# Kernel optimization log

Hardware: AMD Instinct MI355X
Metric: run time of the kernel (lower is better)

Reference implementation:

```python
import jax, jax.numpy as jnp
import numpy as np

N_TAYLOR = 4

def taylor_exp_poly(x, n_terms):
    # sum_{p=0}^{n_terms-1} x^p / p!  via Horner: 1 + x*(1 + x/2*(1 + x/3*(...)))
    acc = jnp.ones_like(x)
    for p in range(n_terms - 1, 0, -1):
        acc = 1.0 + (x / p) * acc
    return acc

def setup_inputs() -> dict:
    key = jax.random.key(0)
    kq, kk, kv = jax.random.split(key, 3)
    B, H, T, d_key, d_val = 4, 8, 2048, 32, 64
    Q = jax.random.normal(kq, (B, H, T, d_key), dtype=jnp.float32)
    K = jax.random.normal(kk, (B, H, T, d_key), dtype=jnp.float32)
    V = jax.random.normal(kv, (B, H, T, d_val), dtype=jnp.float32)
    return {"Q": Q, "K": K, "V": V}

def reference(Q, K, V):
    # Symmetry-aware Taylor-approximated attention (Heinsen & Kozachkov).
    # The tightly-packed degree-p feature maps phi_p satisfy
    #   phi_p(q) . phi_p(k) == (q.k / sqrt(d_key))^p / p!
    # so summing S/Z over all n_taylor terms equals attention with kernel
    #   w(q,k) = sum_{p<n_taylor} (q.k/sqrt(d_key))^p / p!   (truncated exp),
    # causally masked and normalized by the row-sum Z.
    d_key = Q.shape[-1]
    scale = 1.0 / jnp.sqrt(jnp.asarray(d_key, dtype=Q.dtype))
    scores = jnp.einsum('bhqd,bhkd->bhqk', Q, K) * scale  # [B,H,T,T]
    A = taylor_exp_poly(scores, N_TAYLOR)
    T = Q.shape[-2]
    causal = jnp.tril(jnp.ones((T, T), dtype=bool))  # [T,T]
    A = jnp.where(causal, A, jnp.zeros((), dtype=A.dtype))
    Z = jnp.sum(A, axis=-1, keepdims=True)           # [B,H,T,1]
    S = jnp.einsum('bhqk,bhkd->bhqd', A, V)          # [B,H,T,d_val]
    return S / Z
```

## Files before the change

### kernel.cpp

```cpp
#include <hip/hip_runtime.h>
#include <hip/hip_bf16.h>


typedef __attribute__((ext_vector_type(8))) short bf16x8;
typedef __attribute__((ext_vector_type(8))) _Float16 f16x8;
typedef __attribute__((ext_vector_type(2))) _Float16 h2;
typedef __attribute__((ext_vector_type(2))) __fp16 fp16x2b;
typedef __attribute__((ext_vector_type(4))) float f32x4;
typedef __attribute__((ext_vector_type(16))) float f32x16;
typedef unsigned int u32;
typedef unsigned short u16;

namespace {

constexpr int T_SEQ = 2048;
constexpr int DK    = 32;
constexpr int DV    = 64;
constexpr int NBH   = 32;

constexpr float C1 = 0.17677669529663687f;
constexpr float C2 = 0.015625f;
constexpr float C3 = 9.2071195e-4f;

constexpr size_t KHF_OFF  = 0;
constexpr size_t VTHF_OFF = (size_t)NBH * T_SEQ * DK * 2;
constexpr size_t WS_NEED  = VTHF_OFF + (size_t)NBH * DV * T_SEQ * 2;

__device__ __forceinline__ u32 pack_hi2(float f0, float f1) {
  return (__float_as_uint(f0) >> 16) | (__float_as_uint(f1) & 0xffff0000u);
}
__device__ __forceinline__ float trunc_bf(float f) {
  return __uint_as_float(__float_as_uint(f) & 0xffff0000u);
}
__device__ __forceinline__ u16 f2h(float f) {
  union { _Float16 h; u16 u; } c;
  c.h = (_Float16)f;
  return c.u;
}
__device__ __forceinline__ void permswap(u32& a, u32& b) {
  asm volatile("v_permlane32_swap_b32 %0, %1" : "+v"(a), "+v"(b));
}


__global__ void pack_kv(const float* __restrict__ Kg, const float* __restrict__ Vg,
                        u16* __restrict__ Khf, u16* __restrict__ Vthf) {
  __shared__ float tile[DV][33];
  const int bid = blockIdx.x;
  const int t   = threadIdx.x;
  if (bid < 2048) {
    size_t i = ((size_t)bid * 256 + t) * 4;
    float4 f = *(const float4*)(Kg + i);
    ushort4 h;
    h.x = f2h(f.x); h.y = f2h(f.y); h.z = f2h(f.z); h.w = f2h(f.w);
    *(ushort4*)(Khf + i) = h;
  } else {
    const int vb = bid - 2048;
    const int bh = vb >> 6;
    const int k0 = (vb & 63) * 32;
    {
      const int kl = t >> 3, c0 = (t & 7) * 8;
      const float* src = Vg + ((size_t)bh * T_SEQ + k0 + kl) * DV + c0;
      float4 a = *(const float4*)src;
      float4 b = *(const float4*)(src + 4);
      tile[c0 + 0][kl] = a.x; tile[c0 + 1][kl] = a.y;
      tile[c0 + 2][kl] = a.z; tile[c0 + 3][kl] = a.w;
      tile[c0 + 4][kl] = b.x; tile[c0 + 5][kl] = b.y;
      tile[c0 + 6][kl] = b.z; tile[c0 + 7][kl] = b.w;
    }
    __syncthreads();
    {
      const int cl = t >> 2, k8 = (t & 3) * 8;
      ushort4 h0, h1;
      h0.x = f2h(tile[cl][k8 + 0]); h0.y = f2h(tile[cl][k8 + 1]);
      h0.z = f2h(tile[cl][k8 + 2]); h0.w = f2h(tile[cl][k8 + 3]);
      h1.x = f2h(tile[cl][k8 + 4]); h1.y = f2h(tile[cl][k8 + 5]);
      h1.z = f2h(tile[cl][k8 + 6]); h1.w = f2h(tile[cl][k8 + 7]);
      size_t off = ((size_t)(bh * DV + cl)) * T_SEQ + k0 + k8;
      *(ushort4*)(Vthf + off)     = h0;
      *(ushort4*)(Vthf + off + 4) = h1;
    }
  }
}


__global__ __launch_bounds__(256, 4)
void taylor_attn_v10(const float* __restrict__ Qg, const u16* __restrict__ Khf,
                     const u16* __restrict__ Vthf, float* __restrict__ Outg) {
  __shared__ __align__(16) float Sp[4 * 2048];
  __shared__ float Zp[4 * 32];

  const int tid = threadIdx.x;
  const int l   = tid & 63;
  const int w   = tid >> 6;
  const int cq  = l & 31;
  const int hi  = l >> 5;

  const int bid = blockIdx.x;
  const int xcd = bid & 7;
  const int r_  = bid >> 3;
  const int bh  = xcd * 4 + (r_ & 3);
  const int p   = r_ >> 2;

  const u16* kq = Khf + (size_t)bh * T_SEQ * DK + (size_t)cq * DK + hi * 8;
  const u16* vq = Vthf + (size_t)bh * DV * T_SEQ + (size_t)cq * T_SEQ + hi * 8;
  const float* qb = Qg + (size_t)bh * T_SEQ * DK;

  const h2 C3h = {(_Float16)C3, (_Float16)C3};
  const h2 C2h = {(_Float16)C2, (_Float16)C2};
  const h2 C1h = {(_Float16)C1, (_Float16)C1};
  const h2 ONEh = {(_Float16)1.0f, (_Float16)1.0f};

  f32x16 ZERO;
#pragma unroll
  for (int r = 0; r < 16; ++r) ZERO[r] = 0.f;

#pragma unroll 1
  for (int ph = 0; ph < 2; ++ph) {
    const int s  = ph ? (63 - p) : p;
    const int q0 = s * 32;

    if (ph) __syncthreads();

    f16x8 qf[2];
#pragma unroll
    for (int t = 0; t < 2; ++t) {
      const float* qp = qb + (size_t)(q0 + cq) * DK + t * 16 + hi * 8;
      float4 a = *(const float4*)qp;
      float4 b = *(const float4*)(qp + 4);
      f16x8 v;
      v[0] = (_Float16)a.x; v[1] = (_Float16)a.y;
      v[2] = (_Float16)a.z; v[3] = (_Float16)a.w;
      v[4] = (_Float16)b.x; v[5] = (_Float16)b.y;
      v[6] = (_Float16)b.z; v[7] = (_Float16)b.w;
      qf[t] = v;
    }

    f32x16 acc0 = ZERO, acc1 = ZERO;
    float zacc = 0.f;

    auto LOADK = [&](f16x8* kf, int kt) {
      const u16* kp = kq + (size_t)kt * 1024;
      kf[0] = *(const f16x8*)kp;
      kf[1] = *(const f16x8*)(kp + 16);
    };
    auto LOADV = [&](f16x8* vf, int kt) {
#pragma unroll
      for (int ct = 0; ct < 2; ++ct)
#pragma unroll
        for (int t = 0; t < 2; ++t)
          vf[ct * 2 + t] = *(const f16x8*)(
              vq + (size_t)ct * 32 * T_SEQ + kt * 32 + t * 16);
    };
    auto STEP = [&](const f16x8* kf, const f16x8* vf, bool diag) {
      f32x16 d = __builtin_amdgcn_mfma_f32_32x32x16_f16(kf[0], qf[0], ZERO, 0, 0, 0);
      d = __builtin_amdgcn_mfma_f32_32x32x16_f16(kf[1], qf[1], d, 0, 0, 0);

      union cvu { fp16x2b p; h2 h; u32 u; };
      cvu wv[8];
#pragma unroll
      for (int j = 0; j < 8; ++j) {
        cvu c;
        c.p = __builtin_amdgcn_cvt_pkrtz(d[2 * j], d[2 * j + 1]);
        h2 sc = c.h;
        h2 t_ = sc * C3h + C2h;
        t_    = sc * t_ + C1h;
        wv[j].h = sc * t_ + ONEh;
      }
      if (diag) {
#pragma unroll
        for (int j = 0; j < 8; ++j) {
          const int r0   = 2 * j;
          const int kre  = (r0 & 3) + 8 * (r0 >> 2) + 4 * hi;
          u32 msk = ((kre <= cq) ? 0xffffu : 0u) |
                    ((kre + 1 <= cq) ? 0xffff0000u : 0u);
          wv[j].u &= msk;
        }
      }
      {
        h2 zs = ((wv[0].h + wv[1].h) + (wv[2].h + wv[3].h)) +
                ((wv[4].h + wv[5].h) + (wv[6].h + wv[7].h));
        zacc += (float)zs[0] + (float)zs[1];
      }
      union { f16x8 v; u32 u[4]; } WH[2];
#pragma unroll
      for (int t = 0; t < 2; ++t) {
        u32 p0 = wv[4 * t + 0].u, p1 = wv[4 * t + 1].u;
        u32 p2 = wv[4 * t + 2].u, p3 = wv[4 * t + 3].u;
        permswap(p0, p2); permswap(p1, p3);
        WH[t].u[0] = p0; WH[t].u[1] = p1; WH[t].u[2] = p2; WH[t].u[3] = p3;
      }
      acc0 = __builtin_amdgcn_mfma_f32_32x32x16_f16(WH[0].v, vf[0], acc0, 0, 0, 0);
      acc0 = __builtin_amdgcn_mfma_f32_32x32x16_f16(WH[1].v, vf[1], acc0, 0, 0, 0);
      acc1 = __builtin_amdgcn_mfma_f32_32x32x16_f16(WH[0].v, vf[2], acc1, 0, 0, 0);
      acc1 = __builtin_amdgcn_mfma_f32_32x32x16_f16(WH[1].v, vf[3], acc1, 0, 0, 0);
    };

    {
      int kt = w;
      if (kt < s) {
        f16x8 kA[2], kB[2];
        LOADK(kA, kt);
        while (true) {
          int kn = kt + 4;
          if (kn < s) {
            LOADK(kB, kn);
            f16x8 vf[4]; LOADV(vf, kt);
            STEP(kA, vf, false);
            kt = kn;
          } else {
            f16x8 vf[4]; LOADV(vf, kt);
            STEP(kA, vf, false);
            break;
          }
          kn = kt + 4;
          if (kn < s) {
            LOADK(kA, kn);
            f16x8 vf[4]; LOADV(vf, kt);
            STEP(kB, vf, false);
            kt = kn;
          } else {
            f16x8 vf[4]; LOADV(vf, kt);
            STEP(kB, vf, false);
            break;
          }
        }
      }
    }
    if ((s & 3) == w) {
      f16x8 kD[2]; LOADK(kD, s);
      f16x8 vD[4]; LOADV(vD, s);
      STEP(kD, vD, true);
    }

    {
      float zt = zacc + __shfl_xor(zacc, 32);
      if (hi == 0) Zp[w * 32 + cq] = zt;
    }
#pragma unroll
    for (int r = 0; r < 16; ++r) {
      const int qr = (r & 3) + 8 * (r >> 2) + 4 * hi;
      Sp[w * 2048 + qr * 64 + cq]      = acc0[r];
      Sp[w * 2048 + qr * 64 + 32 + cq] = acc1[r];
    }
    __syncthreads();

    const f32x4* S4 = (const f32x4*)Sp;
#pragma unroll
    for (int i = 0; i < 2; ++i) {
      const int e4  = tid + i * 256;
      const int row = e4 >> 4;
      f32x4 ssum = S4[e4] + S4[512 + e4] + S4[1024 + e4] + S4[1536 + e4];
      float z = Zp[row] + Zp[32 + row] + Zp[64 + row] + Zp[96 + row];
      float inv = 1.0f / z;
      float4 o;
      o.x = ssum[0] * inv; o.y = ssum[1] * inv;
      o.z = ssum[2] * inv; o.w = ssum[3] * inv;
      *(float4*)(Outg + ((size_t)bh * T_SEQ + q0 + row) * DV + (e4 & 15) * 4) = o;
    }
  }
}


constexpr int QT_FB = 64;
constexpr int KT_FB = 32;
constexpr int LDSW  = 40;
constexpr float SCALE = 0.17677669529663687f;

__global__ __launch_bounds__(256, 4)
void taylor_attn_fb(const float* __restrict__ Qg, const float* __restrict__ Kg,
                    const float* __restrict__ Vg, float* __restrict__ Outg) {
  __shared__ __align__(16) unsigned short Qhi[QT_FB * LDSW], Qlo[QT_FB * LDSW];
  __shared__ __align__(16) unsigned short Khi_[KT_FB * LDSW], Klo_[KT_FB * LDSW];
  __shared__ __align__(16) unsigned short Vthi_[DV * LDSW], Vtlo_[DV * LDSW];
  __shared__ __align__(16) unsigned Wp[4][16 * 32];

  const int tid  = threadIdx.x;
  const int lane = tid & 63;
  const int wid  = tid >> 6;
  const int m    = lane & 15;
  const int g    = lane >> 4;

  const int bid = blockIdx.x;
  const int v   = bid >> 3;
  const int bh  = (bid & 7) * 4 + (v >> 5);
  const int qt  = 31 - (v & 31);
  const int q0  = qt * QT_FB;

  const float* Qbase = Qg + ((size_t)bh * T_SEQ + q0) * DK;
  const float* Kbase = Kg + (size_t)bh * T_SEQ * DK;
  const float* Vbase = Vg + (size_t)bh * T_SEQ * DV;

#pragma unroll
  for (int p = 0; p < 2; ++p) {
    int e = tid + p * 256, row = e >> 3, c4 = (e & 7) * 4;
    float4 f = *(const float4*)(Qbase + row * DK + c4);
    uint2 h, l;
    h.x = pack_hi2(f.x, f.y); h.y = pack_hi2(f.z, f.w);
    l.x = pack_hi2(f.x - trunc_bf(f.x), f.y - trunc_bf(f.y));
    l.y = pack_hi2(f.z - trunc_bf(f.z), f.w - trunc_bf(f.w));
    *(uint2*)&Qhi[row * LDSW + c4] = h;
    *(uint2*)&Qlo[row * LDSW + c4] = l;
  }
  __syncthreads();

  const int wq = wid * 16;
  const bf16x8 qhi = *(const bf16x8*)&Qhi[(wq + m) * LDSW + g * 8];
  const bf16x8 qlo = *(const bf16x8*)&Qlo[(wq + m) * LDSW + g * 8];

  f32x4 acc[4];
#pragma unroll
  for (int ct = 0; ct < 4; ++ct) acc[ct] = f32x4{0.f, 0.f, 0.f, 0.f};
  float zacc[4] = {0.f, 0.f, 0.f, 0.f};

  const int q_lane0 = q0 + wq + g * 4;
  const int q_wave_max = q0 + wq + 15;

  const int nkt = (q0 + QT_FB) / KT_FB;
  for (int kt = 0; kt < nkt; ++kt) {
    const int k0 = kt * KT_FB;
    __syncthreads();
    {
      int row = tid >> 3, c4 = (tid & 7) * 4;
      float4 f = *(const float4*)(Kbase + (size_t)(k0 + row) * DK + c4);
      uint2 h, l;
      h.x = pack_hi2(f.x, f.y); h.y = pack_hi2(f.z, f.w);
      l.x = pack_hi2(f.x - trunc_bf(f.x), f.y - trunc_bf(f.y));
      l.y = pack_hi2(f.z - trunc_bf(f.z), f.w - trunc_bf(f.w));
      *(uint2*)&Khi_[row * LDSW + c4] = h;
      *(uint2*)&Klo_[row * LDSW + c4] = l;
    }
    {
      int kk = (tid & 15) * 2, c4 = (tid >> 4) * 4;
      const float* vp = Vbase + (size_t)(k0 + kk) * DV + c4;
      float4 a = *(const float4*)vp;
      float4 b = *(const float4*)(vp + DV);
      float af[4] = {a.x, a.y, a.z, a.w};
      float bf_[4] = {b.x, b.y, b.z, b.w};
#pragma unroll
      for (int jj = 0; jj < 4; ++jj) {
        *(unsigned*)&Vthi_[(c4 + jj) * LDSW + kk] = pack_hi2(af[jj], bf_[jj]);
        *(unsigned*)&Vtlo_[(c4 + jj) * LDSW + kk] =
            pack_hi2(af[jj] - trunc_bf(af[jj]), bf_[jj] - trunc_bf(bf_[jj]));
      }
    }
    __syncthreads();

    if (k0 > q_wave_max) continue;

#pragma unroll
    for (int k16 = 0; k16 < 2; ++k16) {
      const int kcol0 = k16 * 16;
      bf16x8 khi = *(const bf16x8*)&Khi_[(kcol0 + m) * LDSW + g * 8];
      bf16x8 klo = *(const bf16x8*)&Klo_[(kcol0 + m) * LDSW + g * 8];
      f32x4 sc = {0.f, 0.f, 0.f, 0.f};
      sc = __builtin_amdgcn_mfma_f32_16x16x32_bf16(qhi, khi, sc, 0, 0, 0);
      sc = __builtin_amdgcn_mfma_f32_16x16x32_bf16(qhi, klo, sc, 0, 0, 0);
      sc = __builtin_amdgcn_mfma_f32_16x16x32_bf16(qlo, khi, sc, 0, 0, 0);
      const int k_abs = k0 + kcol0 + m;
      const int kcol  = kcol0 + m;
#pragma unroll
      for (int r = 0; r < 4; ++r) {
        float x  = sc[r] * SCALE;
        float a3 = __builtin_fmaf(x, 0.3333333333333333f, 1.0f);
        float a2 = __builtin_fmaf(x * 0.5f, a3, 1.0f);
        float wvv = __builtin_fmaf(x, a2, 1.0f);
        wvv = (k_abs <= q_lane0 + r) ? wvv : 0.0f;
        zacc[r] += wvv;
        float wl = wvv - trunc_bf(wvv);
        unsigned packed = (__float_as_uint(wvv) >> 16) |
                          (__float_as_uint(wl) & 0xffff0000u);
        const int q = g * 4 + r;
        Wp[wid][q * 32 + (((kcol >> 2) ^ (q & 7)) << 2) + (kcol & 3)] = packed;
      }
    }

    uint4 pa = *(const uint4*)&Wp[wid][m * 32 + (((2 * g) ^ (m & 7)) << 2)];
    uint4 pb = *(const uint4*)&Wp[wid][m * 32 + (((2 * g + 1) ^ (m & 7)) << 2)];
    union { bf16x8 v; unsigned u[4]; } WH, WL;
    WH.u[0] = (pa.x & 0xffffu) | (pa.y << 16);
    WH.u[1] = (pa.z & 0xffffu) | (pa.w << 16);
    WH.u[2] = (pb.x & 0xffffu) | (pb.y << 16);
    WH.u[3] = (pb.z & 0xffffu) | (pb.w << 16);
    WL.u[0] = (pa.x >> 16) | (pa.y & 0xffff0000u);
    WL.u[1] = (pa.z >> 16) | (pa.w & 0xffff0000u);
    WL.u[2] = (pb.x >> 16) | (pb.y & 0xffff0000u);
    WL.u[3] = (pb.z >> 16) | (pb.w & 0xffff0000u);

#pragma unroll
    for (int ct = 0; ct < 4; ++ct) {
      bf16x8 vhi = *(const bf16x8*)&Vthi_[(ct * 16 + m) * LDSW + g * 8];
      bf16x8 vlo = *(const bf16x8*)&Vtlo_[(ct * 16 + m) * LDSW + g * 8];
      acc[ct] = __builtin_amdgcn_mfma_f32_16x16x32_bf16(WH.v, vhi, acc[ct], 0, 0, 0);
      acc[ct] = __builtin_amdgcn_mfma_f32_16x16x32_bf16(WH.v, vlo, acc[ct], 0, 0, 0);
      acc[ct] = __builtin_amdgcn_mfma_f32_16x16x32_bf16(WL.v, vhi, acc[ct], 0, 0, 0);
    }
  }

  float invz[4];
#pragma unroll
  for (int r = 0; r < 4; ++r) {
    float z = zacc[r];
    z += __shfl_xor(z, 1); z += __shfl_xor(z, 2);
    z += __shfl_xor(z, 4); z += __shfl_xor(z, 8);
    invz[r] = 1.0f / z;
  }

  float* ob = Outg + ((size_t)bh * T_SEQ + (q0 + wq)) * DV;
#pragma unroll
  for (int ct = 0; ct < 4; ++ct)
#pragma unroll
    for (int r = 0; r < 4; ++r)
      ob[(g * 4 + r) * DV + ct * 16 + m] = acc[ct][r] * invz[r];
}

}

extern "C" void kernel_launch(void* const* d_in, const int* in_sizes, int n_in,
                              void* d_out, int out_size, void* d_ws, size_t ws_size,
                              hipStream_t stream) {
  const float* Q = (const float*)d_in[0];
  const float* K = (const float*)d_in[1];
  const float* V = (const float*)d_in[2];
  float* Out = (float*)d_out;

  if (ws_size >= WS_NEED && d_ws != nullptr) {
    u16* khf  = (u16*)((char*)d_ws + KHF_OFF);
    u16* vthf = (u16*)((char*)d_ws + VTHF_OFF);

    hipLaunchKernelGGL(pack_kv, dim3(4096), dim3(256), 0, stream, K, V, khf, vthf);
    hipLaunchKernelGGL(taylor_attn_v10, dim3(1024), dim3(256), 0, stream,
                       Q, khf, vthf, Out);
  } else {
    hipLaunchKernelGGL(taylor_attn_fb, dim3(1024), dim3(256), 0, stream,
                       Q, K, V, Out);
  }
}
```

Baseline: 56.41 us.

## Give each wave its own query tile and drop cross-wave LDS reduction

Before, the four waves of a block split one query tile's key range and reduced partial S and Z through shared memory, with two balanced tiles per block. Now each wave owns a separate 32-row query tile and walks all keys up to the diagonal. The grid halves to 512 blocks, ordered longest-first, and output is normalized directly from registers using a lane shuffle. This removes the LDS reduction and the barriers, at the cost of uneven per-wave work inside a block and less parallelism per query tile.

```diff
diff --git a/kernel.cpp b/kernel.cpp
--- a/kernel.cpp
+++ b/kernel.cpp
@@ -84,11 +84,8 @@
 
 
 __global__ __launch_bounds__(256, 4)
-void taylor_attn_v10(const float* __restrict__ Qg, const u16* __restrict__ Khf,
+void taylor_attn_v13(const float* __restrict__ Qg, const u16* __restrict__ Khf,
                      const u16* __restrict__ Vthf, float* __restrict__ Outg) {
-  __shared__ __align__(16) float Sp[4 * 2048];
-  __shared__ float Zp[4 * 32];
-
   const int tid = threadIdx.x;
   const int l   = tid & 63;
   const int w   = tid >> 6;
@@ -96,14 +93,13 @@
   const int hi  = l >> 5;
 
   const int bid = blockIdx.x;
-  const int xcd = bid & 7;
-  const int r_  = bid >> 3;
-  const int bh  = xcd * 4 + (r_ & 3);
-  const int p   = r_ >> 2;
+  const int t_  = 15 - (bid >> 5);
+  const int bh  = (bid & 7) * 4 + ((bid >> 3) & 3);
+  const int sw  = 4 * t_ + w;
+  const int q0w = sw * 32;
 
   const u16* kq = Khf + (size_t)bh * T_SEQ * DK + (size_t)cq * DK + hi * 8;
   const u16* vq = Vthf + (size_t)bh * DV * T_SEQ + (size_t)cq * T_SEQ + hi * 8;
-  const float* qb = Qg + (size_t)bh * T_SEQ * DK;
 
   const h2 C3h = {(_Float16)C3, (_Float16)C3};
   const h2 C2h = {(_Float16)C2, (_Float16)C2};
@@ -114,149 +110,127 @@
 #pragma unroll
   for (int r = 0; r < 16; ++r) ZERO[r] = 0.f;
 
-#pragma unroll 1
-  for (int ph = 0; ph < 2; ++ph) {
-    const int s  = ph ? (63 - p) : p;
-    const int q0 = s * 32;
-
-    if (ph) __syncthreads();
-
-    f16x8 qf[2];
+  f16x8 qf[2];
+#pragma unroll
+  for (int t = 0; t < 2; ++t) {
+    const float* qp = Qg + ((size_t)bh * T_SEQ + q0w + cq) * DK + t * 16 + hi * 8;
+    float4 a = *(const float4*)qp;
+    float4 b = *(const float4*)(qp + 4);
+    f16x8 v;
+    v[0] = (_Float16)a.x; v[1] = (_Float16)a.y;
+    v[2] = (_Float16)a.z; v[3] = (_Float16)a.w;
+    v[4] = (_Float16)b.x; v[5] = (_Float16)b.y;
+    v[6] = (_Float16)b.z; v[7] = (_Float16)b.w;
+    qf[t] = v;
+  }
+
+  f32x16 acc0 = ZERO, acc1 = ZERO;
+  float zacc = 0.f;
+
+  auto LOADK = [&](f16x8* kf, int kt) {
+    const u16* kp = kq + (size_t)kt * 1024;
+    kf[0] = *(const f16x8*)kp;
+    kf[1] = *(const f16x8*)(kp + 16);
+  };
+  auto LOADV = [&](f16x8* vf, int kt) {
+#pragma unroll
+    for (int ct = 0; ct < 2; ++ct)
+#pragma unroll
+      for (int t = 0; t < 2; ++t)
+        vf[ct * 2 + t] = *(const f16x8*)(
+            vq + (size_t)ct * 32 * T_SEQ + kt * 32 + t * 16);
+  };
+  auto STEP = [&](const f16x8* kf, const f16x8* vf, bool diag) {
+    f32x16 d = __builtin_amdgcn_mfma_f32_32x32x16_f16(kf[0], qf[0], ZERO, 0, 0, 0);
+    d = __builtin_amdgcn_mfma_f32_32x32x16_f16(kf[1], qf[1], d, 0, 0, 0);
+
+    union cvu { fp16x2b p; h2 h; u32 u; };
+    cvu wv[8];
+#pragma unroll
+    for (int j = 0; j < 8; ++j) {
+      cvu c;
+      c.p = __builtin_amdgcn_cvt_pkrtz(d[2 * j], d[2 * j + 1]);
+      h2 sc = c.h;
+      h2 t_h = sc * C3h + C2h;
+      t_h    = sc * t_h + C1h;
+      wv[j].h = sc * t_h + ONEh;
+    }
+    if (diag) {
+#pragma unroll
+      for (int j = 0; j < 8; ++j) {
+        const int r0  = 2 * j;
+        const int kre = (r0 & 3) + 8 * (r0 >> 2) + 4 * hi;
+        u32 msk = ((kre <= cq) ? 0xffffu : 0u) |
+                  ((kre + 1 <= cq) ? 0xffff0000u : 0u);
+        wv[j].u &= msk;
+      }
+    }
+    {
+      h2 zs = ((wv[0].h + wv[1].h) + (wv[2].h + wv[3].h)) +
+              ((wv[4].h + wv[5].h) + (wv[6].h + wv[7].h));
+      zacc += (float)zs[0] + (float)zs[1];
+    }
+    union { f16x8 v; u32 u[4]; } WH[2];
 #pragma unroll
     for (int t = 0; t < 2; ++t) {
-      const float* qp = qb + (size_t)(q0 + cq) * DK + t * 16 + hi * 8;
-      float4 a = *(const float4*)qp;
-      float4 b = *(const float4*)(qp + 4);
-      f16x8 v;
-      v[0] = (_Float16)a.x; v[1] = (_Float16)a.y;
-      v[2] = (_Float16)a.z; v[3] = (_Float16)a.w;
-      v[4] = (_Float16)b.x; v[5] = (_Float16)b.y;
-      v[6] = (_Float16)b.z; v[7] = (_Float16)b.w;
-      qf[t] = v;
-    }
-
-    f32x16 acc0 = ZERO, acc1 = ZERO;
-    float zacc = 0.f;
-
-    auto LOADK = [&](f16x8* kf, int kt) {
-      const u16* kp = kq + (size_t)kt * 1024;
-      kf[0] = *(const f16x8*)kp;
-      kf[1] = *(const f16x8*)(kp + 16);
-    };
-    auto LOADV = [&](f16x8* vf, int kt) {
-#pragma unroll
-      for (int ct = 0; ct < 2; ++ct)
-#pragma unroll
-        for (int t = 0; t < 2; ++t)
-          vf[ct * 2 + t] = *(const f16x8*)(
-              vq + (size_t)ct * 32 * T_SEQ + kt * 32 + t * 16);
-    };
-    auto STEP = [&](const f16x8* kf, const f16x8* vf, bool diag) {
-      f32x16 d = __builtin_amdgcn_mfma_f32_32x32x16_f16(kf[0], qf[0], ZERO, 0, 0, 0);
-      d = __builtin_amdgcn_mfma_f32_32x32x16_f16(kf[1], qf[1], d, 0, 0, 0);
-
-      union cvu { fp16x2b p; h2 h; u32 u; };
-      cvu wv[8];
-#pragma unroll
-      for (int j = 0; j < 8; ++j) {
-        cvu c;
-        c.p = __builtin_amdgcn_cvt_pkrtz(d[2 * j], d[2 * j + 1]);
-        h2 sc = c.h;
-        h2 t_ = sc * C3h + C2h;
-        t_    = sc * t_ + C1h;
-        wv[j].h = sc * t_ + ONEh;
-      }
-      if (diag) {
-#pragma unroll
-        for (int j = 0; j < 8; ++j) {
-          const int r0   = 2 * j;
-          const int kre  = (r0 & 3) + 8 * (r0 >> 2) + 4 * hi;
-          u32 msk = ((kre <= cq) ? 0xffffu : 0u) |
-                    ((kre + 1 <= cq) ? 0xffff0000u : 0u);
-          wv[j].u &= msk;
+      u32 p0 = wv[4 * t + 0].u, p1 = wv[4 * t + 1].u;
+      u32 p2 = wv[4 * t + 2].u, p3 = wv[4 * t + 3].u;
+      permswap(p0, p2); permswap(p1, p3);
+      WH[t].u[0] = p0; WH[t].u[1] = p1; WH[t].u[2] = p2; WH[t].u[3] = p3;
+    }
+    acc0 = __builtin_amdgcn_mfma_f32_32x32x16_f16(WH[0].v, vf[0], acc0, 0, 0, 0);
+    acc0 = __builtin_amdgcn_mfma_f32_32x32x16_f16(WH[1].v, vf[1], acc0, 0, 0, 0);
+    acc1 = __builtin_amdgcn_mfma_f32_32x32x16_f16(WH[0].v, vf[2], acc1, 0, 0, 0);
+    acc1 = __builtin_amdgcn_mfma_f32_32x32x16_f16(WH[1].v, vf[3], acc1, 0, 0, 0);
+  };
+
+  {
+    int kt = 0;
+    if (sw > 0) {
+      f16x8 kA[2], kB[2];
+      LOADK(kA, 0);
+      while (true) {
+        int kn = kt + 1;
+        if (kn < sw) {
+          LOADK(kB, kn);
+          f16x8 vf[4]; LOADV(vf, kt);
+          STEP(kA, vf, false);
+          kt = kn;
+        } else {
+          f16x8 vf[4]; LOADV(vf, kt);
+          STEP(kA, vf, false);
+          break;
+        }
+        kn = kt + 1;
+        if (kn < sw) {
+          LOADK(kA, kn);
+          f16x8 vf[4]; LOADV(vf, kt);
+          STEP(kB, vf, false);
+          kt = kn;
+        } else {
+          f16x8 vf[4]; LOADV(vf, kt);
+          STEP(kB, vf, false);
+          break;
         }
       }
-      {
-        h2 zs = ((wv[0].h + wv[1].h) + (wv[2].h + wv[3].h)) +
-                ((wv[4].h + wv[5].h) + (wv[6].h + wv[7].h));
-        zacc += (float)zs[0] + (float)zs[1];
-      }
-      union { f16x8 v; u32 u[4]; } WH[2];
-#pragma unroll
-      for (int t = 0; t < 2; ++t) {
-        u32 p0 = wv[4 * t + 0].u, p1 = wv[4 * t + 1].u;
-        u32 p2 = wv[4 * t + 2].u, p3 = wv[4 * t + 3].u;
-        permswap(p0, p2); permswap(p1, p3);
-        WH[t].u[0] = p0; WH[t].u[1] = p1; WH[t].u[2] = p2; WH[t].u[3] = p3;
-      }
-      acc0 = __builtin_amdgcn_mfma_f32_32x32x16_f16(WH[0].v, vf[0], acc0, 0, 0, 0);
-      acc0 = __builtin_amdgcn_mfma_f32_32x32x16_f16(WH[1].v, vf[1], acc0, 0, 0, 0);
-      acc1 = __builtin_amdgcn_mfma_f32_32x32x16_f16(WH[0].v, vf[2], acc1, 0, 0, 0);
-      acc1 = __builtin_amdgcn_mfma_f32_32x32x16_f16(WH[1].v, vf[3], acc1, 0, 0, 0);
-    };
-
-    {
-      int kt = w;
-      if (kt < s) {
-        f16x8 kA[2], kB[2];
-        LOADK(kA, kt);
-        while (true) {
-          int kn = kt + 4;
-          if (kn < s) {
-            LOADK(kB, kn);
-            f16x8 vf[4]; LOADV(vf, kt);
-            STEP(kA, vf, false);
-            kt = kn;
-          } else {
-            f16x8 vf[4]; LOADV(vf, kt);
-            STEP(kA, vf, false);
-            break;
-          }
-          kn = kt + 4;
-          if (kn < s) {
-            LOADK(kA, kn);
-            f16x8 vf[4]; LOADV(vf, kt);
-            STEP(kB, vf, false);
-            kt = kn;
-          } else {
-            f16x8 vf[4]; LOADV(vf, kt);
-            STEP(kB, vf, false);
-            break;
-          }
-        }
-      }
-    }
-    if ((s & 3) == w) {
-      f16x8 kD[2]; LOADK(kD, s);
-      f16x8 vD[4]; LOADV(vD, s);
-      STEP(kD, vD, true);
-    }
-
-    {
-      float zt = zacc + __shfl_xor(zacc, 32);
-      if (hi == 0) Zp[w * 32 + cq] = zt;
-    }
-#pragma unroll
-    for (int r = 0; r < 16; ++r) {
-      const int qr = (r & 3) + 8 * (r >> 2) + 4 * hi;
-      Sp[w * 2048 + qr * 64 + cq]      = acc0[r];
-      Sp[w * 2048 + qr * 64 + 32 + cq] = acc1[r];
-    }
-    __syncthreads();
-
-    const f32x4* S4 = (const f32x4*)Sp;
-#pragma unroll
-    for (int i = 0; i < 2; ++i) {
-      const int e4  = tid + i * 256;
-      const int row = e4 >> 4;
-      f32x4 ssum = S4[e4] + S4[512 + e4] + S4[1024 + e4] + S4[1536 + e4];
-      float z = Zp[row] + Zp[32 + row] + Zp[64 + row] + Zp[96 + row];
-      float inv = 1.0f / z;
-      float4 o;
-      o.x = ssum[0] * inv; o.y = ssum[1] * inv;
-      o.z = ssum[2] * inv; o.w = ssum[3] * inv;
-      *(float4*)(Outg + ((size_t)bh * T_SEQ + q0 + row) * DV + (e4 & 15) * 4) = o;
-    }
+    }
+  }
+  {
+    f16x8 kD[2]; LOADK(kD, sw);
+    f16x8 vD[4]; LOADV(vD, sw);
+    STEP(kD, vD, true);
+  }
+
+  float zt = zacc + __shfl_xor(zacc, 32);
+  float iz = 1.0f / zt;
+
+  float* ob = Outg + ((size_t)bh * T_SEQ + q0w) * DV;
+#pragma unroll
+  for (int r = 0; r < 16; ++r) {
+    const int qr = (r & 3) + 8 * (r >> 2) + 4 * hi;
+    float izr = __shfl(iz, qr);
+    ob[(size_t)qr * DV + cq]      = acc0[r] * izr;
+    ob[(size_t)qr * DV + 32 + cq] = acc1[r] * izr;
   }
 }
 
@@ -428,7 +402,7 @@
     u16* vthf = (u16*)((char*)d_ws + VTHF_OFF);
 
     hipLaunchKernelGGL(pack_kv, dim3(4096), dim3(256), 0, stream, K, V, khf, vthf);
-    hipLaunchKernelGGL(taylor_attn_v10, dim3(1024), dim3(256), 0, stream,
+    hipLaunchKernelGGL(taylor_attn_v13, dim3(512), dim3(256), 0, stream,
                        Q, khf, vthf, Out);
   } else {
     hipLaunchKernelGGL(taylor_attn_fb, dim3(1024), dim3(256), 0, stream,
```

Result: slower. 68.69 us (+21.8%).
